# Kernel tuning notes

Measured on AMD Instinct MI355X. Metric: run time of the kernel, lower is better.

Reference implementation:

```python
import math
import jax, jax.numpy as jnp
import numpy as np

B, T, C = 1, 4096, 1024
H, DH = 16, 64
BAND = 128

def setup_inputs() -> dict:
    key = jax.random.key(0)
    ks = jax.random.split(key, 5)
    scale = 0.02
    return {
        "x":  jax.random.normal(ks[0], (B, T, C), dtype=jnp.float32),
        "Wq": jax.random.normal(ks[1], (C, C), dtype=jnp.float32) * scale,
        "Wk": jax.random.normal(ks[2], (C, C), dtype=jnp.float32) * scale,
        "Wv": jax.random.normal(ks[3], (C, C), dtype=jnp.float32) * scale,
        "Wo": jax.random.normal(ks[4], (C, C), dtype=jnp.float32) * scale,
    }

def _band_causal_mask(T, band, dtype=jnp.bool_):
    # allowed iff j <= i and (i - j) < band
    i = jnp.arange(T)[:, None]
    j = jnp.arange(T)[None, :]
    return (j <= i) & ((i - j) < band)  # (T, T)

def reference(x, Wq, Wk, Wv, Wo):
    Bs, Ts, Cs = x.shape
    # nn.Linear: y = x @ W^T (bias=False)
    q = (x @ Wq.T).reshape(Bs, Ts, H, DH).transpose(0, 2, 1, 3)  # (B,H,T,Dh)
    k = (x @ Wk.T).reshape(Bs, Ts, H, DH).transpose(0, 2, 1, 3)
    v = (x @ Wv.T).reshape(Bs, Ts, H, DH).transpose(0, 2, 1, 3)
    att = jnp.einsum('bhid,bhjd->bhij', q, k) / math.sqrt(DH)      # (B,H,T,T)
    mask = _band_causal_mask(Ts, BAND)                              # (T,T)
    att = jnp.where(mask[None, None], att, jnp.finfo(att.dtype).min)
    P = jax.nn.softmax(att, axis=-1)
    y = jnp.einsum('bhij,bhjd->bhid', P, v)                         # (B,H,T,Dh)
    y = y.transpose(0, 2, 1, 3).reshape(Bs, Ts, Cs)                 # (B,T,C)
    return y @ Wo.T
```

## Files before the change

### kernel.cpp

```cpp
#include <hip/hip_runtime.h>
#include <hip/hip_bf16.h>
#include <stdint.h>

#define T_SEQ 4096
#define CDIM  1024
#define NH    16
#define DHEAD 64
#define BAND  128

typedef __bf16 bf16;
typedef __attribute__((ext_vector_type(8)))  __bf16 bf16x8;
typedef __attribute__((ext_vector_type(4)))  __bf16 bf16x4;
typedef __attribute__((ext_vector_type(4)))  float  f32x4;
typedef __attribute__((ext_vector_type(16))) float  f32x16;

#define QSCALE 0.1803368801111204f

__device__ __forceinline__ void async_ld16(const bf16* g, bf16* l) {
    __builtin_amdgcn_global_load_lds(
        (__attribute__((address_space(1))) void*)g,
        (__attribute__((address_space(3))) void*)l, 16, 0, 0);
}

__global__ void cvt_all(const float* __restrict__ x,  const float* __restrict__ wq,
                        const float* __restrict__ wk, const float* __restrict__ wv,
                        bf16* __restrict__ xb, bf16* __restrict__ wqkvb) {
    size_t g = (size_t)blockIdx.x * 256 + threadIdx.x;
    const float* s; bf16* d;
    if (g < 524288) {
        s = x + g * 8; d = xb + g * 8;
    } else {
        size_t i2 = (g - 524288) * 8;
        int which = (int)(i2 >> 20);
        s = ((which == 0) ? wq : (which == 1) ? wk : wv) + (i2 & 1048575);
        d = wqkvb + i2;
    }
    const float4* sv = (const float4*)s;
    float4 a = sv[0], b = sv[1];
    bf16x8 o;
    o[0] = (bf16)a.x; o[1] = (bf16)a.y; o[2] = (bf16)a.z; o[3] = (bf16)a.w;
    o[4] = (bf16)b.x; o[5] = (bf16)b.y; o[6] = (bf16)b.z; o[7] = (bf16)b.w;
    *(bf16x8*)d = o;
}

__global__ __launch_bounds__(256) void gemm_qkv(
        const bf16* __restrict__ A, const bf16* __restrict__ B,
        bf16* __restrict__ qb, bf16* __restrict__ kb, bf16* __restrict__ vtb) {
    const int K = 1024;
    __shared__ __align__(16) bf16 lds_a[128 * 64];
    __shared__ __align__(16) bf16 lds_b[128 * 64];
    int t = threadIdx.x;
    int w = t >> 6, l = t & 63;
    int e31 = l & 31, h2 = l >> 5;
    int bx = blockIdx.x;
    int bm = bx & 31, bn = bx >> 5;
    int m0 = bm * 128, n0 = bn * 128;
    int wm = (w >> 1) * 64, wn = (w & 1) * 64;

    f32x16 acc[2][2];
#pragma unroll
    for (int i = 0; i < 2; i++)
#pragma unroll
        for (int j = 0; j < 2; j++)
#pragma unroll
            for (int r = 0; r < 16; r++) acc[i][j][r] = 0.f;

    int row_s[4], ko_s[4];
#pragma unroll
    for (int it = 0; it < 4; it++) {
        int cid = it * 256 + t;
        row_s[it] = cid >> 3;
        ko_s[it] = ((cid & 7) ^ (row_s[it] & 7)) * 8;
    }
    int rowa0 = wm + e31, rowa1 = wm + 32 + e31;
    int rowb0 = wn + e31, rowb1 = wn + 32 + e31;
    int sa0 = rowa0 & 7, sa1 = rowa1 & 7, sb0 = rowb0 & 7, sb1 = rowb1 & 7;
    const bf16* ba0 = lds_a + rowa0 * 64;
    const bf16* ba1 = lds_a + rowa1 * 64;
    const bf16* bb0 = lds_b + rowb0 * 64;
    const bf16* bb1 = lds_b + rowb1 * 64;

    for (int k0 = 0; k0 < K; k0 += 64) {
#pragma unroll
        for (int it = 0; it < 4; it++) {
            bf16* dst_a = lds_a + (it * 256 + w * 64) * 8;
            bf16* dst_b = lds_b + (it * 256 + w * 64) * 8;
            async_ld16(A + (size_t)(m0 + row_s[it]) * K + k0 + ko_s[it], dst_a);
            async_ld16(B + (size_t)(n0 + row_s[it]) * K + k0 + ko_s[it], dst_b);
        }
        __syncthreads();
#pragma unroll
        for (int kk = 0; kk < 4; kk++) {
            int lc = kk * 2 + h2;
            bf16x8 a0 = *(const bf16x8*)(ba0 + ((lc ^ sa0) * 8));
            bf16x8 a1 = *(const bf16x8*)(ba1 + ((lc ^ sa1) * 8));
            bf16x8 b0 = *(const bf16x8*)(bb0 + ((lc ^ sb0) * 8));
            bf16x8 b1 = *(const bf16x8*)(bb1 + ((lc ^ sb1) * 8));
            acc[0][0] = __builtin_amdgcn_mfma_f32_32x32x16_bf16(a0, b0, acc[0][0], 0, 0, 0);
            acc[0][1] = __builtin_amdgcn_mfma_f32_32x32x16_bf16(a0, b1, acc[0][1], 0, 0, 0);
            acc[1][0] = __builtin_amdgcn_mfma_f32_32x32x16_bf16(a1, b0, acc[1][0], 0, 0, 0);
            acc[1][1] = __builtin_amdgcn_mfma_f32_32x32x16_bf16(a1, b1, acc[1][1], 0, 0, 0);
        }
        __syncthreads();
    }

    if (n0 < 2048) {
        bool isQ = (n0 < 1024);
        bf16* dst = isQ ? qb : kb;
        float scale = isQ ? QSCALE : 1.0f;
        int obase = n0 & 1023;
#pragma unroll
        for (int i = 0; i < 2; i++)
#pragma unroll
            for (int j = 0; j < 2; j++) {
                int o = obase + wn + j * 32 + e31;
                int h = o >> 6, d = o & 63;
#pragma unroll
                for (int r = 0; r < 16; r++) {
                    int trow = m0 + wm + i * 32 + (r & 3) + 8 * (r >> 2) + 4 * h2;
                    dst[((size_t)(h * T_SEQ + trow)) * 64 + d] = (bf16)(acc[i][j][r] * scale);
                }
            }
    } else {
        int obase = n0 - 2048;
#pragma unroll
        for (int i = 0; i < 2; i++)
#pragma unroll
            for (int j = 0; j < 2; j++) {
                int o = obase + wn + j * 32 + e31;
                size_t base = (size_t)o * T_SEQ;
#pragma unroll
                for (int rq = 0; rq < 4; rq++) {
                    int tbase = m0 + wm + i * 32 + 8 * rq + 4 * h2;
                    bf16x4 pk;
#pragma unroll
                    for (int rr = 0; rr < 4; rr++) pk[rr] = (bf16)acc[i][j][rq * 4 + rr];
                    *(bf16x4*)(vtb + base + tbase) = pk;
                }
            }
    }
}

#define PSTR 168

__global__ __launch_bounds__(256) void attn(
        const bf16* __restrict__ qbuf, const bf16* __restrict__ kbuf,
        const bf16* __restrict__ vtbuf, bf16* __restrict__ yb,
        const float* __restrict__ wo, bf16* __restrict__ wob) {
    __shared__ __align__(16) bf16 p_lds[4 * 32 * PSTR];
    int t = threadIdx.x;
    int w = t >> 6, l = t & 63;
    int quad = l >> 4, col = l & 15;

    {
        size_t g = ((size_t)blockIdx.x * 256 + t) * 8;
        const float4* sv = (const float4*)(wo + g);
        float4 a = sv[0], b = sv[1];
        bf16x8 o8;
        o8[0] = (bf16)a.x; o8[1] = (bf16)a.y; o8[2] = (bf16)a.z; o8[3] = (bf16)a.w;
        o8[4] = (bf16)b.x; o8[5] = (bf16)b.y; o8[6] = (bf16)b.z; o8[7] = (bf16)b.w;
        *(bf16x8*)(wob + g) = o8;
    }

    int h = blockIdx.x >> 5;
    int qt = blockIdx.x & 31;
    int i0 = qt * 128;
    int rowbase = i0 + w * 32;
    int jbase = rowbase - 128;

    const bf16* Q  = qbuf  + (size_t)h * T_SEQ * 64;
    const bf16* Kp = kbuf  + (size_t)h * T_SEQ * 64;
    const bf16* Vt = vtbuf + (size_t)h * 64 * T_SEQ;

    bf16x8 qf[2][2];
#pragma unroll
    for (int mi = 0; mi < 2; mi++)
#pragma unroll
        for (int kk = 0; kk < 2; kk++)
            qf[mi][kk] = *(const bf16x8*)(Q + (size_t)(rowbase + mi * 16 + col) * 64 + kk * 32 + quad * 8);

    f32x4 s[2][10];
#pragma unroll
    for (int mi = 0; mi < 2; mi++)
#pragma unroll
        for (int nj = 0; nj < 10; nj++) s[mi][nj] = (f32x4){0.f, 0.f, 0.f, 0.f};
#pragma unroll
    for (int nj = 0; nj < 10; nj++) {
        int jr = jbase + nj * 16 + col;
        int jl = jr < 0 ? 0 : jr;
#pragma unroll
        for (int kk = 0; kk < 2; kk++) {
            bf16x8 kf = *(const bf16x8*)(Kp + (size_t)jl * 64 + kk * 32 + quad * 8);
#pragma unroll
            for (int mi = 0; mi < 2; mi++)
                s[mi][nj] = __builtin_amdgcn_mfma_f32_16x16x32_bf16(qf[mi][kk], kf, s[mi][nj], 0, 0, 0);
        }
    }

    float l_run[2][4];
#pragma unroll
    for (int mi = 0; mi < 2; mi++)
#pragma unroll
        for (int r = 0; r < 4; r++) {
            int ii = rowbase + mi * 16 + quad * 4 + r;
            float rs = 0.f;
#pragma unroll
            for (int nj = 0; nj < 10; nj++) {
                int jj = jbase + nj * 16 + col;
                bool ok = (jj >= 0) && ((unsigned)(ii - jj) < (unsigned)BAND);
                float p = ok ? __builtin_amdgcn_exp2f(s[mi][nj][r]) : 0.f;
                s[mi][nj][r] = p;
                rs += p;
            }
            rs += __shfl_xor(rs, 1);
            rs += __shfl_xor(rs, 2);
            rs += __shfl_xor(rs, 4);
            rs += __shfl_xor(rs, 8);
            l_run[mi][r] = rs;
        }

    bf16* myp = p_lds + (size_t)w * (32 * PSTR);
#pragma unroll
    for (int mi = 0; mi < 2; mi++)
#pragma unroll
        for (int nj = 0; nj < 10; nj++)
#pragma unroll
            for (int r = 0; r < 4; r++)
                myp[(mi * 16 + quad * 4 + r) * PSTR + nj * 16 + col] = (bf16)s[mi][nj][r];

    f32x4 o_acc[2][4];
#pragma unroll
    for (int mi = 0; mi < 2; mi++)
#pragma unroll
        for (int di = 0; di < 4; di++) o_acc[mi][di] = (f32x4){0.f, 0.f, 0.f, 0.f};
#pragma unroll
    for (int kj = 0; kj < 5; kj++) {
        int jv = jbase + kj * 32 + quad * 8;
        int jvc = jv < 0 ? 0 : jv;
        bf16x8 pf[2];
#pragma unroll
        for (int mi = 0; mi < 2; mi++)
            pf[mi] = *(const bf16x8*)(myp + (mi * 16 + col) * PSTR + kj * 32 + quad * 8);
#pragma unroll
        for (int di = 0; di < 4; di++) {
            bf16x8 vf = *(const bf16x8*)(Vt + (size_t)(di * 16 + col) * T_SEQ + jvc);
#pragma unroll
            for (int mi = 0; mi < 2; mi++)
                o_acc[mi][di] = __builtin_amdgcn_mfma_f32_16x16x32_bf16(pf[mi], vf, o_acc[mi][di], 0, 0, 0);
        }
    }

#pragma unroll
    for (int mi = 0; mi < 2; mi++)
#pragma unroll
        for (int di = 0; di < 4; di++)
#pragma unroll
            for (int r = 0; r < 4; r++) {
                int tt = rowbase + mi * 16 + quad * 4 + r;
                int c = h * 64 + di * 16 + col;
                yb[(size_t)tt * CDIM + c] = (bf16)(o_acc[mi][di][r] / l_run[mi][r]);
            }
}

__global__ __launch_bounds__(256) void gemm_proj(
        const bf16* __restrict__ A, const bf16* __restrict__ B,
        float* __restrict__ Cout) {
    const int K = 1024;
    __shared__ __align__(16) bf16 lds_a[64 * 64];
    __shared__ __align__(16) bf16 lds_b[128 * 64];
    int t = threadIdx.x;
    int w = t >> 6, l = t & 63;
    int e31 = l & 31, h2 = l >> 5;
    int bx = blockIdx.x;
    int bm = bx & 63, bn = bx >> 6;
    int m0 = bm * 64, n0 = bn * 128;
    int wm = (w >> 1) * 32, wn = (w & 1) * 64;

    f32x16 acc[2];
#pragma unroll
    for (int j = 0; j < 2; j++)
#pragma unroll
        for (int r = 0; r < 16; r++) acc[j][r] = 0.f;

    int rowA[2], koA[2], rowB[4], koB[4];
#pragma unroll
    for (int it = 0; it < 2; it++) {
        int cid = it * 256 + t;
        rowA[it] = cid >> 3;
        koA[it] = ((cid & 7) ^ (rowA[it] & 7)) * 8;
    }
#pragma unroll
    for (int it = 0; it < 4; it++) {
        int cid = it * 256 + t;
        rowB[it] = cid >> 3;
        koB[it] = ((cid & 7) ^ (rowB[it] & 7)) * 8;
    }
    int rowa = wm + e31;
    int rowb0 = wn + e31, rowb1 = wn + 32 + e31;
    int sa = rowa & 7, sb0 = rowb0 & 7, sb1 = rowb1 & 7;
    const bf16* ba = lds_a + rowa * 64;
    const bf16* bb0 = lds_b + rowb0 * 64;
    const bf16* bb1 = lds_b + rowb1 * 64;

    for (int k0 = 0; k0 < K; k0 += 64) {
#pragma unroll
        for (int it = 0; it < 2; it++)
            async_ld16(A + (size_t)(m0 + rowA[it]) * K + k0 + koA[it],
                       lds_a + (it * 256 + w * 64) * 8);
#pragma unroll
        for (int it = 0; it < 4; it++)
            async_ld16(B + (size_t)(n0 + rowB[it]) * K + k0 + koB[it],
                       lds_b + (it * 256 + w * 64) * 8);
        __syncthreads();
#pragma unroll
        for (int kk = 0; kk < 4; kk++) {
            int lc = kk * 2 + h2;
            bf16x8 af = *(const bf16x8*)(ba + ((lc ^ sa) * 8));
            bf16x8 b0 = *(const bf16x8*)(bb0 + ((lc ^ sb0) * 8));
            bf16x8 b1 = *(const bf16x8*)(bb1 + ((lc ^ sb1) * 8));
            acc[0] = __builtin_amdgcn_mfma_f32_32x32x16_bf16(af, b0, acc[0], 0, 0, 0);
            acc[1] = __builtin_amdgcn_mfma_f32_32x32x16_bf16(af, b1, acc[1], 0, 0, 0);
        }
        __syncthreads();
    }
#pragma unroll
    for (int j = 0; j < 2; j++) {
        int ncol = n0 + wn + j * 32 + e31;
#pragma unroll
        for (int r = 0; r < 16; r++) {
            int trow = m0 + wm + (r & 3) + 8 * (r >> 2) + 4 * h2;
            Cout[(size_t)trow * CDIM + ncol] = acc[j][r];
        }
    }
}

extern "C" void kernel_launch(void* const* d_in, const int* in_sizes, int n_in,
                              void* d_out, int out_size, void* d_ws, size_t ws_size,
                              hipStream_t stream) {
    const float* x  = (const float*)d_in[0];
    const float* Wq = (const float*)d_in[1];
    const float* Wk = (const float*)d_in[2];
    const float* Wv = (const float*)d_in[3];
    const float* Wo = (const float*)d_in[4];
    float* out = (float*)d_out;

    char* ws = (char*)d_ws;
    bf16* xb    = (bf16*)(ws);
    bf16* wqkvb = (bf16*)(ws + ((size_t)8  << 20));
    bf16* wob   = (bf16*)(ws + ((size_t)14 << 20));
    bf16* qb    = (bf16*)(ws + ((size_t)16 << 20));
    bf16* kb    = (bf16*)(ws + ((size_t)24 << 20));
    bf16* vtb   = (bf16*)(ws + ((size_t)32 << 20));
    bf16* yb    = (bf16*)(ws + ((size_t)40 << 20));

    cvt_all<<<3584, 256, 0, stream>>>(x, Wq, Wk, Wv, xb, wqkvb);
    gemm_qkv<<<768, 256, 0, stream>>>(xb, wqkvb, qb, kb, vtb);
    attn<<<512, 256, 0, stream>>>(qb, kb, vtb, yb, Wo, wob);
    gemm_proj<<<512, 256, 0, stream>>>(yb, wob, out);
}
```

Measured before the change: 144.6 us.

## Halve attention rows per wave and double attention grid to 1024 blocks

The attention kernel now gives each wave 16 query rows instead of 32, with 64 rows per block, and launches 1024 blocks instead of 512. The key range per wave shrinks from 10 to 9 tiles of 16, which avoids computing a fully masked tile, and the unused LDS tail columns are zero-filled for the PV step. This raises parallelism and occupancy and cuts wasted QK work, at the cost of reloading each K/V band in more blocks. The Wo conversion is restricted to the first 512 blocks.

After: 152.2 us. +5.3%, slower.

```diff
diff --git a/kernel.cpp b/kernel.cpp
--- a/kernel.cpp
+++ b/kernel.cpp
@@ -147,12 +147,12 @@
         const bf16* __restrict__ qbuf, const bf16* __restrict__ kbuf,
         const bf16* __restrict__ vtbuf, bf16* __restrict__ yb,
         const float* __restrict__ wo, bf16* __restrict__ wob) {
-    __shared__ __align__(16) bf16 p_lds[4 * 32 * PSTR];
+    __shared__ __align__(16) bf16 p_lds[4 * 16 * PSTR];
     int t = threadIdx.x;
     int w = t >> 6, l = t & 63;
     int quad = l >> 4, col = l & 15;
 
-    {
+    if (blockIdx.x < 512) {
         size_t g = ((size_t)blockIdx.x * 256 + t) * 8;
         const float4* sv = (const float4*)(wo + g);
         float4 a = sv[0], b = sv[1];
@@ -162,104 +162,89 @@
         *(bf16x8*)(wob + g) = o8;
     }
 
-    int h = blockIdx.x >> 5;
-    int qt = blockIdx.x & 31;
-    int i0 = qt * 128;
-    int rowbase = i0 + w * 32;
+    int h = blockIdx.x >> 6;
+    int qt = blockIdx.x & 63;
+    int i0 = qt * 64;
+    int rowbase = i0 + w * 16;
     int jbase = rowbase - 128;
 
     const bf16* Q  = qbuf  + (size_t)h * T_SEQ * 64;
     const bf16* Kp = kbuf  + (size_t)h * T_SEQ * 64;
     const bf16* Vt = vtbuf + (size_t)h * 64 * T_SEQ;
 
-    bf16x8 qf[2][2];
-#pragma unroll
-    for (int mi = 0; mi < 2; mi++)
-#pragma unroll
-        for (int kk = 0; kk < 2; kk++)
-            qf[mi][kk] = *(const bf16x8*)(Q + (size_t)(rowbase + mi * 16 + col) * 64 + kk * 32 + quad * 8);
-
-    f32x4 s[2][10];
-#pragma unroll
-    for (int mi = 0; mi < 2; mi++)
-#pragma unroll
-        for (int nj = 0; nj < 10; nj++) s[mi][nj] = (f32x4){0.f, 0.f, 0.f, 0.f};
-#pragma unroll
-    for (int nj = 0; nj < 10; nj++) {
+    bf16x8 qf[2];
+#pragma unroll
+    for (int kk = 0; kk < 2; kk++)
+        qf[kk] = *(const bf16x8*)(Q + (size_t)(rowbase + col) * 64 + kk * 32 + quad * 8);
+
+    f32x4 s[9];
+#pragma unroll
+    for (int nj = 0; nj < 9; nj++) s[nj] = (f32x4){0.f, 0.f, 0.f, 0.f};
+#pragma unroll
+    for (int nj = 0; nj < 9; nj++) {
         int jr = jbase + nj * 16 + col;
         int jl = jr < 0 ? 0 : jr;
 #pragma unroll
         for (int kk = 0; kk < 2; kk++) {
             bf16x8 kf = *(const bf16x8*)(Kp + (size_t)jl * 64 + kk * 32 + quad * 8);
-#pragma unroll
-            for (int mi = 0; mi < 2; mi++)
-                s[mi][nj] = __builtin_amdgcn_mfma_f32_16x16x32_bf16(qf[mi][kk], kf, s[mi][nj], 0, 0, 0);
-        }
-    }
-
-    float l_run[2][4];
-#pragma unroll
-    for (int mi = 0; mi < 2; mi++)
-#pragma unroll
-        for (int r = 0; r < 4; r++) {
-            int ii = rowbase + mi * 16 + quad * 4 + r;
-            float rs = 0.f;
-#pragma unroll
-            for (int nj = 0; nj < 10; nj++) {
-                int jj = jbase + nj * 16 + col;
-                bool ok = (jj >= 0) && ((unsigned)(ii - jj) < (unsigned)BAND);
-                float p = ok ? __builtin_amdgcn_exp2f(s[mi][nj][r]) : 0.f;
-                s[mi][nj][r] = p;
-                rs += p;
-            }
-            rs += __shfl_xor(rs, 1);
-            rs += __shfl_xor(rs, 2);
-            rs += __shfl_xor(rs, 4);
-            rs += __shfl_xor(rs, 8);
-            l_run[mi][r] = rs;
-        }
-
-    bf16* myp = p_lds + (size_t)w * (32 * PSTR);
-#pragma unroll
-    for (int mi = 0; mi < 2; mi++)
-#pragma unroll
-        for (int nj = 0; nj < 10; nj++)
-#pragma unroll
-            for (int r = 0; r < 4; r++)
-                myp[(mi * 16 + quad * 4 + r) * PSTR + nj * 16 + col] = (bf16)s[mi][nj][r];
-
-    f32x4 o_acc[2][4];
-#pragma unroll
-    for (int mi = 0; mi < 2; mi++)
-#pragma unroll
-        for (int di = 0; di < 4; di++) o_acc[mi][di] = (f32x4){0.f, 0.f, 0.f, 0.f};
+            s[nj] = __builtin_amdgcn_mfma_f32_16x16x32_bf16(qf[kk], kf, s[nj], 0, 0, 0);
+        }
+    }
+
+    float l_run[4];
+#pragma unroll
+    for (int r = 0; r < 4; r++) {
+        int ii = rowbase + quad * 4 + r;
+        float rs = 0.f;
+#pragma unroll
+        for (int nj = 0; nj < 9; nj++) {
+            int jj = jbase + nj * 16 + col;
+            bool ok = (jj >= 0) && ((unsigned)(ii - jj) < (unsigned)BAND);
+            float p = ok ? __builtin_amdgcn_exp2f(s[nj][r]) : 0.f;
+            s[nj][r] = p;
+            rs += p;
+        }
+        rs += __shfl_xor(rs, 1);
+        rs += __shfl_xor(rs, 2);
+        rs += __shfl_xor(rs, 4);
+        rs += __shfl_xor(rs, 8);
+        l_run[r] = rs;
+    }
+
+    bf16* myp = p_lds + w * (16 * PSTR);
+#pragma unroll
+    for (int nj = 0; nj < 9; nj++)
+#pragma unroll
+        for (int r = 0; r < 4; r++)
+            myp[(quad * 4 + r) * PSTR + nj * 16 + col] = (bf16)s[nj][r];
+    {
+        int zr = l >> 2, zc = 144 + (l & 3) * 4;
+        *(bf16x4*)(myp + zr * PSTR + zc) = (bf16x4){(bf16)0.f, (bf16)0.f, (bf16)0.f, (bf16)0.f};
+    }
+
+    f32x4 o_acc[4];
+#pragma unroll
+    for (int di = 0; di < 4; di++) o_acc[di] = (f32x4){0.f, 0.f, 0.f, 0.f};
 #pragma unroll
     for (int kj = 0; kj < 5; kj++) {
         int jv = jbase + kj * 32 + quad * 8;
         int jvc = jv < 0 ? 0 : jv;
-        bf16x8 pf[2];
-#pragma unroll
-        for (int mi = 0; mi < 2; mi++)
-            pf[mi] = *(const bf16x8*)(myp + (mi * 16 + col) * PSTR + kj * 32 + quad * 8);
+        bf16x8 pf = *(const bf16x8*)(myp + col * PSTR + kj * 32 + quad * 8);
 #pragma unroll
         for (int di = 0; di < 4; di++) {
             bf16x8 vf = *(const bf16x8*)(Vt + (size_t)(di * 16 + col) * T_SEQ + jvc);
-#pragma unroll
-            for (int mi = 0; mi < 2; mi++)
-                o_acc[mi][di] = __builtin_amdgcn_mfma_f32_16x16x32_bf16(pf[mi], vf, o_acc[mi][di], 0, 0, 0);
-        }
-    }
-
-#pragma unroll
-    for (int mi = 0; mi < 2; mi++)
-#pragma unroll
-        for (int di = 0; di < 4; di++)
-#pragma unroll
-            for (int r = 0; r < 4; r++) {
-                int tt = rowbase + mi * 16 + quad * 4 + r;
-                int c = h * 64 + di * 16 + col;
-                yb[(size_t)tt * CDIM + c] = (bf16)(o_acc[mi][di][r] / l_run[mi][r]);
-            }
+            o_acc[di] = __builtin_amdgcn_mfma_f32_16x16x32_bf16(pf, vf, o_acc[di], 0, 0, 0);
+        }
+    }
+
+#pragma unroll
+    for (int di = 0; di < 4; di++)
+#pragma unroll
+        for (int r = 0; r < 4; r++) {
+            int tt = rowbase + quad * 4 + r;
+            int c = h * 64 + di * 16 + col;
+            yb[(size_t)tt * CDIM + c] = (bf16)(o_acc[di][r] / l_run[r]);
+        }
 }
 
 __global__ __launch_bounds__(256) void gemm_proj(
@@ -355,6 +340,6 @@
 
     cvt_all<<<3584, 256, 0, stream>>>(x, Wq, Wk, Wv, xb, wqkvb);
     gemm_qkv<<<768, 256, 0, stream>>>(xb, wqkvb, qb, kb, vtb);
-    attn<<<512, 256, 0, stream>>>(qb, kb, vtb, yb, Wo, wob);
+    attn<<<1024, 256, 0, stream>>>(qb, kb, vtb, yb, Wo, wob);
     gemm_proj<<<512, 256, 0, stream>>>(yb, wob, out);
 }
```
